# Kernel optimization log

Measured on AMD Instinct MI355X. Metric: run time of the kernel, lower is better.

Reference implementation:

```python
import jax, jax.numpy as jnp
import numpy as np

B, S, H, I = 2, 2048, 4096, 14336

def setup_inputs() -> dict:
    key = jax.random.key(0)
    k1, k2, k3, k4 = jax.random.split(key, 4)
    sH = 1.0 / np.sqrt(H)
    sI = 1.0 / np.sqrt(I)
    return {
        "x": jax.random.normal(k1, (B, S, H), dtype=jnp.float32),
        "w_gate": jax.random.normal(k2, (I, H), dtype=jnp.float32) * sH,
        "w_up": jax.random.normal(k3, (I, H), dtype=jnp.float32) * sH,
        "w_down": jax.random.normal(k4, (H, I), dtype=jnp.float32) * sI,
    }

def reference(x, w_gate, w_up, w_down):
    # SwiGLU gated MLP: down( silu(x @ Wg^T) * (x @ Wu^T) )
    g = jnp.einsum("bsh,ih->bsi", x, w_gate)   # [B,S,I]
    u = jnp.einsum("bsh,ih->bsi", x, w_up)     # [B,S,I]
    a = jax.nn.silu(g) * u                      # fused silu_mul
    d = jnp.einsum("bsi,hi->bsh", a, w_down)   # [B,S,H]
    return d
```

## Files before the change

kernel.cpp:

```cpp
#include <hip/hip_runtime.h>
#include <hip/hip_bf16.h>
#include <stdint.h>

typedef __bf16 bf16_t;
typedef __bf16 bf16x4 __attribute__((ext_vector_type(4)));
typedef __bf16 bf16x8 __attribute__((ext_vector_type(8)));
typedef float f32x4 __attribute__((ext_vector_type(4)));

#define LDS_CAST(p) ((__attribute__((address_space(3))) void*)(p))
#define GLB_CAST(p) ((const __attribute__((address_space(1))) void*)(p))

__device__ __forceinline__ void gl_lds16(const void* g, void* l) {
  __builtin_amdgcn_global_load_lds(GLB_CAST(g), LDS_CAST(l), 16, 0, 0);
}

#define MFMA16(a,b,c) __builtin_amdgcn_mfma_f32_16x16x32_bf16((a),(b),(c),0,0,0)
#define BARRIER() __builtin_amdgcn_s_barrier()

template<int N> __device__ __forceinline__ void vmw() {
  if constexpr (N == 8)      asm volatile("s_waitcnt vmcnt(8)" ::: "memory");
  else if constexpr (N == 6) asm volatile("s_waitcnt vmcnt(6)" ::: "memory");
  else if constexpr (N == 4) asm volatile("s_waitcnt vmcnt(4)" ::: "memory");
  else if constexpr (N == 0) asm volatile("s_waitcnt vmcnt(0)" ::: "memory");
}

static constexpr int M_TOT = 4096, H_DIM = 4096, I_DIM = 14336;

__global__ __launch_bounds__(256)
void k_conv(const float4* __restrict__ src, bf16x4* __restrict__ dst, long n4)
{
  long stride = (long)gridDim.x * blockDim.x;
  for (long i = (long)blockIdx.x * blockDim.x + threadIdx.x; i < n4; i += stride) {
    float4 v = src[i];
    bf16x4 o;
    o[0] = (bf16_t)v.x; o[1] = (bf16_t)v.y; o[2] = (bf16_t)v.z; o[3] = (bf16_t)v.w;
    dst[i] = o;
  }
}

__global__ __launch_bounds__(512, 2)
void k_gateup8(const bf16_t* __restrict__ X, const bf16_t* __restrict__ Wg,
               const bf16_t* __restrict__ Wu, bf16_t* __restrict__ Aout)
{
  __shared__ __align__(1024) char lds[131072];
  const int tid = threadIdx.x, wave = tid >> 6, lane = tid & 63;
  const int lr = lane & 15, kg = lane >> 4;
  const int xm = ((lr >> 3) & 1) << 5;
  const int wm = wave >> 2, wn = wave & 3;

  const int bid = blockIdx.x;
  const int i8  = bid >> 3;
  const int tn  = (bid & 7) * 14 + (i8 >> 4);
  const int tm  = i8 & 15;

  const int srow  = tid >> 2;
  const int scolb = ((tid & 3) * 16) ^ (((tid >> 5) & 1) << 5);

  const bf16_t* gX = X  + (size_t)(tm * 256 + srow) * H_DIM + (scolb >> 1);
  const bf16_t* gG = Wg + (size_t)(tn * 128 + srow) * H_DIM + (scolb >> 1);
  const bf16_t* gU = Wu + (size_t)(tn * 128 + srow) * H_DIM + (scolb >> 1);
  const size_t xh = (size_t)128 * H_DIM;

  const int ck   = (kg * 16) ^ xm;
  const int offA = (wm * 128 + lr) * 64 + ck;
  const int offG = 16384 + (wn * 32 + lr) * 64 + ck;
  const int offU = offG + 8192;

  const f32x4 vz = {0.f, 0.f, 0.f, 0.f};
  f32x4 accg[8][2], accu[8][2];
#pragma unroll
  for (int m = 0; m < 8; ++m)
#pragma unroll
    for (int n = 0; n < 2; ++n) { accg[m][n] = vz; accu[m][n] = vz; }

#pragma unroll
  for (int t = 0; t < 3; ++t) {
    char* lb = lds + t * 32768 + wave * 1024;
    gl_lds16(gX + t * 32,      lb);
    gl_lds16(gX + xh + t * 32, lb + 8192);
    gl_lds16(gG + t * 32,      lb + 16384);
    gl_lds16(gU + t * 32,      lb + 24576);
  }
  vmw<8>(); BARRIER();

#define G1_TILE(T, DO_STG, WAITN, DO_BAR)                                    \
  {                                                                          \
    const char* bb = lds + (((T) & 3) << 15);                                \
    if (DO_STG) {                                                            \
      char* sb = lds + ((((T) + 3) & 3) << 15) + wave * 1024;                \
      const int kc = ((T) + 3) * 32;                                         \
      gl_lds16(gX + kc,      sb);                                            \
      gl_lds16(gX + xh + kc, sb + 8192);                                     \
      gl_lds16(gG + kc,      sb + 16384);                                    \
      gl_lds16(gU + kc,      sb + 24576);                                    \
    }                                                                        \
    bf16x8 bg[2], bu[2], a[8];                                               \
    _Pragma("unroll") for (int n = 0; n < 2; ++n) {                          \
      bg[n] = *(const bf16x8*)(bb + offG + n * 1024);                        \
      bu[n] = *(const bf16x8*)(bb + offU + n * 1024); }                      \
    _Pragma("unroll") for (int f = 0; f < 8; ++f)                            \
      a[f] = *(const bf16x8*)(bb + offA + f * 1024);                         \
    __builtin_amdgcn_s_setprio(1);                                           \
    _Pragma("unroll") for (int m = 0; m < 8; ++m)                            \
    _Pragma("unroll") for (int n = 0; n < 2; ++n) {                          \
      accg[m][n] = MFMA16(a[m], bg[n], accg[m][n]);                          \
      accu[m][n] = MFMA16(a[m], bu[n], accu[m][n]); }                        \
    __builtin_amdgcn_s_setprio(0);                                           \
    vmw<WAITN>();                                                            \
    if (DO_BAR) BARRIER();                                                   \
  }

  const int NT = H_DIM / 32;
  for (int T = 0; T <= NT - 4; ++T)
    G1_TILE(T, true, 6, true);
  G1_TILE(NT - 3, false, 4, true);
  G1_TILE(NT - 2, false, 0, true);
  G1_TILE(NT - 1, false, 8 , false);
#undef G1_TILE

  const int r0 = tm * 256 + wm * 128 + kg * 4;
  const int c0 = tn * 128 + wn * 32 + lr;
#pragma unroll
  for (int m = 0; m < 8; ++m)
#pragma unroll
    for (int n = 0; n < 2; ++n)
#pragma unroll
      for (int e = 0; e < 4; ++e) {
        float g = accg[m][n][e];
        float u = accu[m][n][e];
        float s = g / (1.0f + __expf(-g));
        Aout[(size_t)(r0 + m * 16 + e) * I_DIM + c0 + n * 16] = (bf16_t)(s * u);
      }
}

__global__ __launch_bounds__(512, 2)
void k_down8(const bf16_t* __restrict__ Aa, const bf16_t* __restrict__ Wd,
             float* __restrict__ D)
{
  __shared__ __align__(1024) char lds[131072];
  const int tid = threadIdx.x, wave = tid >> 6, lane = tid & 63;
  const int lr = lane & 15, kg = lane >> 4;
  const int xm = ((lr >> 3) & 1) << 5;
  const int wm = wave >> 2, wn = wave & 3;

  const int bid = blockIdx.x;
  const int i8  = bid >> 3;
  const int tn  = (bid & 7) * 2 + (i8 >> 4);
  const int tm  = i8 & 15;

  const int srow  = tid >> 2;
  const int scolb = ((tid & 3) * 16) ^ (((tid >> 5) & 1) << 5);

  const bf16_t* gA = Aa + (size_t)(tm * 256 + srow) * I_DIM + (scolb >> 1);
  const bf16_t* gB = Wd + (size_t)(tn * 256 + srow) * I_DIM + (scolb >> 1);
  const size_t hI = (size_t)128 * I_DIM;

  const int ck   = (kg * 16) ^ xm;
  const int offA = (wm * 128 + lr) * 64 + ck;
  const int offB = 16384 + (wn * 64 + lr) * 64 + ck;

  const f32x4 vz = {0.f, 0.f, 0.f, 0.f};
  f32x4 acc[8][4];
#pragma unroll
  for (int m = 0; m < 8; ++m)
#pragma unroll
    for (int n = 0; n < 4; ++n) acc[m][n] = vz;

#pragma unroll
  for (int t = 0; t < 3; ++t) {
    char* lb = lds + t * 32768 + wave * 1024;
    gl_lds16(gA + t * 32,      lb);
    gl_lds16(gA + hI + t * 32, lb + 8192);
    gl_lds16(gB + t * 32,      lb + 16384);
    gl_lds16(gB + hI + t * 32, lb + 24576);
  }
  vmw<8>(); BARRIER();

#define G2_TILE(T, DO_STG, WAITN, DO_BAR)                                    \
  {                                                                          \
    const char* bb = lds + (((T) & 3) << 15);                                \
    if (DO_STG) {                                                            \
      char* sb = lds + ((((T) + 3) & 3) << 15) + wave * 1024;                \
      const int kc = ((T) + 3) * 32;                                         \
      gl_lds16(gA + kc,      sb);                                            \
      gl_lds16(gA + hI + kc, sb + 8192);                                     \
      gl_lds16(gB + kc,      sb + 16384);                                    \
      gl_lds16(gB + hI + kc, sb + 24576);                                    \
    }                                                                        \
    bf16x8 b[4], a[8];                                                       \
    _Pragma("unroll") for (int n = 0; n < 4; ++n)                            \
      b[n] = *(const bf16x8*)(bb + offB + n * 1024);                         \
    _Pragma("unroll") for (int f = 0; f < 8; ++f)                            \
      a[f] = *(const bf16x8*)(bb + offA + f * 1024);                         \
    __builtin_amdgcn_s_setprio(1);                                           \
    _Pragma("unroll") for (int m = 0; m < 8; ++m)                            \
    _Pragma("unroll") for (int n = 0; n < 4; ++n)                            \
      acc[m][n] = MFMA16(a[m], b[n], acc[m][n]);                             \
    __builtin_amdgcn_s_setprio(0);                                           \
    vmw<WAITN>();                                                            \
    if (DO_BAR) BARRIER();                                                   \
  }

  const int NT = I_DIM / 32;
  for (int T = 0; T <= NT - 4; ++T)
    G2_TILE(T, true, 6, true);
  G2_TILE(NT - 3, false, 4, true);
  G2_TILE(NT - 2, false, 0, true);
  G2_TILE(NT - 1, false, 8, false);
#undef G2_TILE

  const int r0 = tm * 256 + wm * 128 + kg * 4;
  const int c0 = tn * 256 + wn * 64 + lr;
#pragma unroll
  for (int m = 0; m < 8; ++m)
#pragma unroll
    for (int n = 0; n < 4; ++n)
#pragma unroll
      for (int e = 0; e < 4; ++e)
        D[(size_t)(r0 + m * 16 + e) * H_DIM + c0 + n * 16] = acc[m][n][e];
}

extern "C" void kernel_launch(void* const* d_in, const int* in_sizes, int n_in,
                              void* d_out, int out_size, void* d_ws, size_t ws_size,
                              hipStream_t stream) {
  const float* x  = (const float*)d_in[0];
  const float* wg = (const float*)d_in[1];
  const float* wu = (const float*)d_in[2];
  const float* wd = (const float*)d_in[3];
  float* out = (float*)d_out;

  const size_t A_BYTES = (size_t)M_TOT * I_DIM * 2;
  const size_t X_BYTES = (size_t)M_TOT * H_DIM * 2;
  const size_t W_BYTES = (size_t)I_DIM * H_DIM * 2;
  char* ws = (char*)d_ws;
  bf16_t* Ab  = (bf16_t*)(ws);
  bf16_t* Xb  = (bf16_t*)(ws + A_BYTES);
  bf16_t* Wgb = (bf16_t*)(ws + A_BYTES + X_BYTES);
  bf16_t* Wub = (bf16_t*)(ws + A_BYTES + X_BYTES + W_BYTES);
  bf16_t* Wdb = Wgb;

  const long nX = (long)M_TOT * H_DIM / 4;
  const long nW = (long)I_DIM * H_DIM / 4;

  k_conv<<<dim3(2048), dim3(256), 0, stream>>>((const float4*)x,  (bf16x4*)Xb,  nX);
  k_conv<<<dim3(2048), dim3(256), 0, stream>>>((const float4*)wg, (bf16x4*)Wgb, nW);
  k_conv<<<dim3(2048), dim3(256), 0, stream>>>((const float4*)wu, (bf16x4*)Wub, nW);

  k_gateup8<<<dim3(16 * 112), dim3(512), 0, stream>>>(Xb, Wgb, Wub, Ab);

  k_conv<<<dim3(2048), dim3(256), 0, stream>>>((const float4*)wd, (bf16x4*)Wdb, nW);

  k_down8<<<dim3(16 * 16), dim3(512), 0, stream>>>(Ab, Wdb, out);
}
```

Before: 1.439 ms.

## Double-buffer LDS fragment reads in registers to overlap with MFMA

Both GEMM kernels now keep two register sets of operand fragments. The LDS reads for the next k-tile are issued before the MFMAs of the current tile, with the main loop unrolled by two and the global-to-LDS staging rescheduled around it. This is meant to hide LDS read latency behind matrix-core work instead of stalling on reads just before the MFMAs. It uses more VGPRs, which could cause spills or lower occupancy under the 512x2 launch bounds.

```diff
diff --git a/kernel.cpp b/kernel.cpp
--- a/kernel.cpp
+++ b/kernel.cpp
@@ -16,10 +16,10 @@
 
 #define MFMA16(a,b,c) __builtin_amdgcn_mfma_f32_16x16x32_bf16((a),(b),(c),0,0,0)
 #define BARRIER() __builtin_amdgcn_s_barrier()
+#define PRIO(n)  __builtin_amdgcn_s_setprio(n)
 
 template<int N> __device__ __forceinline__ void vmw() {
   if constexpr (N == 8)      asm volatile("s_waitcnt vmcnt(8)" ::: "memory");
-  else if constexpr (N == 6) asm volatile("s_waitcnt vmcnt(6)" ::: "memory");
   else if constexpr (N == 4) asm volatile("s_waitcnt vmcnt(4)" ::: "memory");
   else if constexpr (N == 0) asm volatile("s_waitcnt vmcnt(0)" ::: "memory");
 }
@@ -39,7 +39,7 @@
 }
 
 __global__ __launch_bounds__(512, 2)
-void k_gateup8(const bf16_t* __restrict__ X, const bf16_t* __restrict__ Wg,
+void k_gateup9(const bf16_t* __restrict__ X, const bf16_t* __restrict__ Wg,
                const bf16_t* __restrict__ Wu, bf16_t* __restrict__ Aout)
 {
   __shared__ __align__(1024) char lds[131072];
@@ -47,11 +47,12 @@
   const int lr = lane & 15, kg = lane >> 4;
   const int xm = ((lr >> 3) & 1) << 5;
   const int wm = wave >> 2, wn = wave & 3;
+  const int wb = wave * 1024;
 
   const int bid = blockIdx.x;
-  const int i8  = bid >> 3;
-  const int tn  = (bid & 7) * 14 + (i8 >> 4);
-  const int tm  = i8 & 15;
+  const int bq  = bid >> 3;
+  const int tn  = (bid & 7) * 14 + (bq >> 4);
+  const int tm  = bq & 15;
 
   const int srow  = tid >> 2;
   const int scolb = ((tid & 3) * 16) ^ (((tid >> 5) & 1) << 5);
@@ -73,50 +74,55 @@
 #pragma unroll
     for (int n = 0; n < 2; ++n) { accg[m][n] = vz; accu[m][n] = vz; }
 
-#pragma unroll
-  for (int t = 0; t < 3; ++t) {
-    char* lb = lds + t * 32768 + wave * 1024;
-    gl_lds16(gX + t * 32,      lb);
-    gl_lds16(gX + xh + t * 32, lb + 8192);
-    gl_lds16(gG + t * 32,      lb + 16384);
-    gl_lds16(gU + t * 32,      lb + 24576);
-  }
-  vmw<8>(); BARRIER();
-
-#define G1_TILE(T, DO_STG, WAITN, DO_BAR)                                    \
-  {                                                                          \
-    const char* bb = lds + (((T) & 3) << 15);                                \
-    if (DO_STG) {                                                            \
-      char* sb = lds + ((((T) + 3) & 3) << 15) + wave * 1024;                \
-      const int kc = ((T) + 3) * 32;                                         \
-      gl_lds16(gX + kc,      sb);                                            \
-      gl_lds16(gX + xh + kc, sb + 8192);                                     \
-      gl_lds16(gG + kc,      sb + 16384);                                    \
-      gl_lds16(gU + kc,      sb + 24576);                                    \
-    }                                                                        \
-    bf16x8 bg[2], bu[2], a[8];                                               \
+#define G1_STAGE(TT)                                                         \
+  { char* sb = lds + (((TT) & 3) << 15) + wb;                                \
+    const int kc = (TT) * 32;                                                \
+    gl_lds16(gX + kc,      sb);                                              \
+    gl_lds16(gX + xh + kc, sb + 8192);                                       \
+    gl_lds16(gG + kc,      sb + 16384);                                      \
+    gl_lds16(gU + kc,      sb + 24576); }
+
+#define G1_READS(SET, TT)                                                    \
+  { const char* rb = lds + (((TT) & 3) << 15);                               \
+    _Pragma("unroll") for (int f = 0; f < 8; ++f)                            \
+      a##SET[f] = *(const bf16x8*)(rb + offA + f * 1024);                    \
     _Pragma("unroll") for (int n = 0; n < 2; ++n) {                          \
-      bg[n] = *(const bf16x8*)(bb + offG + n * 1024);                        \
-      bu[n] = *(const bf16x8*)(bb + offU + n * 1024); }                      \
-    _Pragma("unroll") for (int f = 0; f < 8; ++f)                            \
-      a[f] = *(const bf16x8*)(bb + offA + f * 1024);                         \
-    __builtin_amdgcn_s_setprio(1);                                           \
+      bg##SET[n] = *(const bf16x8*)(rb + offG + n * 1024);                   \
+      bu##SET[n] = *(const bf16x8*)(rb + offU + n * 1024); } }
+
+#define G1_MFMA(SET)                                                         \
+  { PRIO(1);                                                                 \
     _Pragma("unroll") for (int m = 0; m < 8; ++m)                            \
     _Pragma("unroll") for (int n = 0; n < 2; ++n) {                          \
-      accg[m][n] = MFMA16(a[m], bg[n], accg[m][n]);                          \
-      accu[m][n] = MFMA16(a[m], bu[n], accu[m][n]); }                        \
-    __builtin_amdgcn_s_setprio(0);                                           \
-    vmw<WAITN>();                                                            \
-    if (DO_BAR) BARRIER();                                                   \
+      accg[m][n] = MFMA16(a##SET[m], bg##SET[n], accg[m][n]);                \
+      accu[m][n] = MFMA16(a##SET[m], bu##SET[n], accu[m][n]); }              \
+    PRIO(0); }
+
+  bf16x8 aA[8], bgA[2], buA[2];
+  bf16x8 aB[8], bgB[2], buB[2];
+
+  G1_STAGE(0); G1_STAGE(1); G1_STAGE(2);
+  vmw<8>(); BARRIER();
+  G1_READS(A, 0);
+
+  const int NT = H_DIM / 32;
+  for (int T = 0; T < NT - 4; T += 2) {
+    vmw<4>(); BARRIER();
+    G1_READS(B, T + 1);
+    G1_STAGE(T + 3);
+    G1_MFMA(A);
+    vmw<4>(); BARRIER();
+    G1_READS(A, T + 2);
+    G1_STAGE(T + 4);
+    G1_MFMA(B);
   }
-
-  const int NT = H_DIM / 32;
-  for (int T = 0; T <= NT - 4; ++T)
-    G1_TILE(T, true, 6, true);
-  G1_TILE(NT - 3, false, 4, true);
-  G1_TILE(NT - 2, false, 0, true);
-  G1_TILE(NT - 1, false, 8 , false);
-#undef G1_TILE
+  vmw<4>(); BARRIER(); G1_READS(B, NT - 3); G1_STAGE(NT - 1); G1_MFMA(A);
+  vmw<4>(); BARRIER(); G1_READS(A, NT - 2);                   G1_MFMA(B);
+  vmw<0>(); BARRIER(); G1_READS(B, NT - 1);                   G1_MFMA(A);
+  G1_MFMA(B);
+#undef G1_STAGE
+#undef G1_READS
+#undef G1_MFMA
 
   const int r0 = tm * 256 + wm * 128 + kg * 4;
   const int c0 = tn * 128 + wn * 32 + lr;
@@ -134,7 +140,7 @@
 }
 
 __global__ __launch_bounds__(512, 2)
-void k_down8(const bf16_t* __restrict__ Aa, const bf16_t* __restrict__ Wd,
+void k_down9(const bf16_t* __restrict__ Aa, const bf16_t* __restrict__ Wd,
              float* __restrict__ D)
 {
   __shared__ __align__(1024) char lds[131072];
@@ -142,11 +148,12 @@
   const int lr = lane & 15, kg = lane >> 4;
   const int xm = ((lr >> 3) & 1) << 5;
   const int wm = wave >> 2, wn = wave & 3;
+  const int wb = wave * 1024;
 
   const int bid = blockIdx.x;
-  const int i8  = bid >> 3;
-  const int tn  = (bid & 7) * 2 + (i8 >> 4);
-  const int tm  = i8 & 15;
+  const int bq  = bid >> 3;
+  const int tn  = (bid & 7) * 2 + (bq >> 4);
+  const int tm  = bq & 15;
 
   const int srow  = tid >> 2;
   const int scolb = ((tid & 3) * 16) ^ (((tid >> 5) & 1) << 5);
@@ -166,48 +173,53 @@
 #pragma unroll
     for (int n = 0; n < 4; ++n) acc[m][n] = vz;
 
-#pragma unroll
-  for (int t = 0; t < 3; ++t) {
-    char* lb = lds + t * 32768 + wave * 1024;
-    gl_lds16(gA + t * 32,      lb);
-    gl_lds16(gA + hI + t * 32, lb + 8192);
-    gl_lds16(gB + t * 32,      lb + 16384);
-    gl_lds16(gB + hI + t * 32, lb + 24576);
-  }
-  vmw<8>(); BARRIER();
-
-#define G2_TILE(T, DO_STG, WAITN, DO_BAR)                                    \
-  {                                                                          \
-    const char* bb = lds + (((T) & 3) << 15);                                \
-    if (DO_STG) {                                                            \
-      char* sb = lds + ((((T) + 3) & 3) << 15) + wave * 1024;                \
-      const int kc = ((T) + 3) * 32;                                         \
-      gl_lds16(gA + kc,      sb);                                            \
-      gl_lds16(gA + hI + kc, sb + 8192);                                     \
-      gl_lds16(gB + kc,      sb + 16384);                                    \
-      gl_lds16(gB + hI + kc, sb + 24576);                                    \
-    }                                                                        \
-    bf16x8 b[4], a[8];                                                       \
+#define G2_STAGE(TT)                                                         \
+  { char* sb = lds + (((TT) & 3) << 15) + wb;                                \
+    const int kc = (TT) * 32;                                                \
+    gl_lds16(gA + kc,      sb);                                              \
+    gl_lds16(gA + hI + kc, sb + 8192);                                       \
+    gl_lds16(gB + kc,      sb + 16384);                                      \
+    gl_lds16(gB + hI + kc, sb + 24576); }
+
+#define G2_READS(SET, TT)                                                    \
+  { const char* rb = lds + (((TT) & 3) << 15);                               \
+    _Pragma("unroll") for (int f = 0; f < 8; ++f)                            \
+      a##SET[f] = *(const bf16x8*)(rb + offA + f * 1024);                    \
     _Pragma("unroll") for (int n = 0; n < 4; ++n)                            \
-      b[n] = *(const bf16x8*)(bb + offB + n * 1024);                         \
-    _Pragma("unroll") for (int f = 0; f < 8; ++f)                            \
-      a[f] = *(const bf16x8*)(bb + offA + f * 1024);                         \
-    __builtin_amdgcn_s_setprio(1);                                           \
+      b##SET[n] = *(const bf16x8*)(rb + offB + n * 1024); }
+
+#define G2_MFMA(SET)                                                         \
+  { PRIO(1);                                                                 \
     _Pragma("unroll") for (int m = 0; m < 8; ++m)                            \
     _Pragma("unroll") for (int n = 0; n < 4; ++n)                            \
-      acc[m][n] = MFMA16(a[m], b[n], acc[m][n]);                             \
-    __builtin_amdgcn_s_setprio(0);                                           \
-    vmw<WAITN>();                                                            \
-    if (DO_BAR) BARRIER();                                                   \
+      acc[m][n] = MFMA16(a##SET[m], b##SET[n], acc[m][n]);                   \
+    PRIO(0); }
+
+  bf16x8 aA[8], bA[4];
+  bf16x8 aB[8], bB[4];
+
+  G2_STAGE(0); G2_STAGE(1); G2_STAGE(2);
+  vmw<8>(); BARRIER();
+  G2_READS(A, 0);
+
+  const int NT = I_DIM / 32;
+  for (int T = 0; T < NT - 4; T += 2) {
+    vmw<4>(); BARRIER();
+    G2_READS(B, T + 1);
+    G2_STAGE(T + 3);
+    G2_MFMA(A);
+    vmw<4>(); BARRIER();
+    G2_READS(A, T + 2);
+    G2_STAGE(T + 4);
+    G2_MFMA(B);
   }
-
-  const int NT = I_DIM / 32;
-  for (int T = 0; T <= NT - 4; ++T)
-    G2_TILE(T, true, 6, true);
-  G2_TILE(NT - 3, false, 4, true);
-  G2_TILE(NT - 2, false, 0, true);
-  G2_TILE(NT - 1, false, 8, false);
-#undef G2_TILE
+  vmw<4>(); BARRIER(); G2_READS(B, NT - 3); G2_STAGE(NT - 1); G2_MFMA(A);
+  vmw<4>(); BARRIER(); G2_READS(A, NT - 2);                   G2_MFMA(B);
+  vmw<0>(); BARRIER(); G2_READS(B, NT - 1);                   G2_MFMA(A);
+  G2_MFMA(B);
+#undef G2_STAGE
+#undef G2_READS
+#undef G2_MFMA
 
   const int r0 = tm * 256 + wm * 128 + kg * 4;
   const int c0 = tn * 256 + wn * 64 + lr;
@@ -246,9 +258,9 @@
   k_conv<<<dim3(2048), dim3(256), 0, stream>>>((const float4*)wg, (bf16x4*)Wgb, nW);
   k_conv<<<dim3(2048), dim3(256), 0, stream>>>((const float4*)wu, (bf16x4*)Wub, nW);
 
-  k_gateup8<<<dim3(16 * 112), dim3(512), 0, stream>>>(Xb, Wgb, Wub, Ab);
+  k_gateup9<<<dim3(16 * 112), dim3(512), 0, stream>>>(Xb, Wgb, Wub, Ab);
 
   k_conv<<<dim3(2048), dim3(256), 0, stream>>>((const float4*)wd, (bf16x4*)Wdb, nW);
 
-  k_down8<<<dim3(16 * 16), dim3(512), 0, stream>>>(Ab, Wdb, out);
-}
+  k_down9<<<dim3(16 * 16), dim3(512), 0, stream>>>(Ab, Wdb, out);
+}
```

Result: no change. 1.418 ms (-1.5%).
